# Performance work log

Hardware: AMD Instinct MI355X
Metric: run time of the kernel (lower is better)

The kernel has to match this reference:

```python
import jax, jax.numpy as jnp
import numpy as np

IM_SIZE = (32, 32)
SCALE = float(IM_SIZE[0] * IM_SIZE[1])  # sqrt((x*y)^2) = x*y


def setup_inputs() -> dict:
    key = jax.random.key(0)
    k1, k2, k3 = jax.random.split(key, 3)
    b, n, p, x, y, d = 8, 8, 64, IM_SIZE[0], IM_SIZE[1], 8
    shape = (b, n, p, x, y, d)
    return {
        "query": jax.random.normal(k1, shape, dtype=jnp.float32),
        "key": jax.random.normal(k2, shape, dtype=jnp.float32),
        "value": jax.random.normal(k3, shape, dtype=jnp.float32),
        "key_padding_mask": jnp.zeros((b, p), dtype=bool),
    }


def reference(query, key, value, key_padding_mask):
    # scores: contract over spatial (x,y) and channel (d) dims -> [b,n,p,q]
    scores = jnp.einsum('bnpxyd,bnqxyd->bnpq', query, key) / SCALE
    if key_padding_mask is not None:
        mask = key_padding_mask[:, None, None, :]  # [b,1,1,q]
        scores = jnp.where(mask, -jnp.inf, scores)
    attn = jax.nn.softmax(scores, axis=-1)  # [b,n,p,q]
    out = jnp.einsum('bnpq,bnqxyd->bnpxyd', attn, value)
    # permute(0,2,3,4,5,1) -> [b,p,x,y,d,n]
    return jnp.transpose(out, (0, 2, 3, 4, 5, 1))
```

## Files before the change

### kernel.cpp

```cpp
#include <hip/hip_runtime.h>
#include <hip/hip_bf16.h>
#include <cstdint>
#include <cstddef>


typedef __attribute__((ext_vector_type(4))) float f32x4;
typedef __attribute__((ext_vector_type(8))) short bf16x8;
typedef __attribute__((ext_vector_type(4))) short shortx4;

__device__ __forceinline__ unsigned short f2bf(float x) {
    unsigned int u = __builtin_bit_cast(unsigned int, x);
    u += 0x7FFFu + ((u >> 16) & 1u);
    return (unsigned short)(u >> 16);
}

#define BKK 32
#define LDS_STRIDE 68

__global__ __launch_bounds__(256) void qk_partial_kernel(
    const float* __restrict__ Q, const float* __restrict__ K,
    float* __restrict__ partial, int clen)
{
    __shared__ float As[BKK][LDS_STRIDE];
    __shared__ float Bs[BKK][LDS_STRIDE];
    const int bn  = blockIdx.x;
    const int ch  = blockIdx.y;
    const int tid = threadIdx.x;
    const float* Qb = Q + (size_t)bn * 64 * 8192;
    const float* Kb = K + (size_t)bn * 64 * 8192;
    const int k0 = ch * clen;

    const int lp  = tid >> 2;
    const int lk0 = (tid & 3) * 4;
    const int r0 = (tid >> 4) * 4;
    const int c0 = (tid & 15) * 4;

    float acc[4][4];
    #pragma unroll
    for (int i = 0; i < 4; ++i)
        #pragma unroll
        for (int j = 0; j < 4; ++j) acc[i][j] = 0.f;

    for (int kb = 0; kb < clen; kb += BKK) {
        const int kbase = k0 + kb;
        const float4 qa = *(const float4*)&Qb[(size_t)lp * 8192 + kbase + lk0];
        const float4 qc = *(const float4*)&Qb[(size_t)lp * 8192 + kbase + lk0 + 16];
        const float4 ka = *(const float4*)&Kb[(size_t)lp * 8192 + kbase + lk0];
        const float4 kc = *(const float4*)&Kb[(size_t)lp * 8192 + kbase + lk0 + 16];
        __syncthreads();
        As[lk0 + 0][lp] = qa.x;  As[lk0 + 1][lp] = qa.y;
        As[lk0 + 2][lp] = qa.z;  As[lk0 + 3][lp] = qa.w;
        As[lk0 + 16][lp] = qc.x; As[lk0 + 17][lp] = qc.y;
        As[lk0 + 18][lp] = qc.z; As[lk0 + 19][lp] = qc.w;
        Bs[lk0 + 0][lp] = ka.x;  Bs[lk0 + 1][lp] = ka.y;
        Bs[lk0 + 2][lp] = ka.z;  Bs[lk0 + 3][lp] = ka.w;
        Bs[lk0 + 16][lp] = kc.x; Bs[lk0 + 17][lp] = kc.y;
        Bs[lk0 + 18][lp] = kc.z; Bs[lk0 + 19][lp] = kc.w;
        __syncthreads();
        #pragma unroll
        for (int kk = 0; kk < BKK; ++kk) {
            const float4 av = *(const float4*)&As[kk][r0];
            const float4 bv = *(const float4*)&Bs[kk][c0];
            const float a4[4] = {av.x, av.y, av.z, av.w};
            const float b4[4] = {bv.x, bv.y, bv.z, bv.w};
            #pragma unroll
            for (int i = 0; i < 4; ++i)
                #pragma unroll
                for (int j = 0; j < 4; ++j)
                    acc[i][j] = fmaf(a4[i], b4[j], acc[i][j]);
        }
    }

    float* pb = partial + (((size_t)ch * 64 + bn) * 64) * 64;
    #pragma unroll
    for (int i = 0; i < 4; ++i) {
        float4 v;
        v.x = acc[i][0]; v.y = acc[i][1]; v.z = acc[i][2]; v.w = acc[i][3];
        *(float4*)&pb[(size_t)(r0 + i) * 64 + c0] = v;
    }
}

__global__ __launch_bounds__(256) void softmax_kernel(
    float* __restrict__ ws, const unsigned char* __restrict__ mask, int kchunks)
{
    const int row  = blockIdx.x * 4 + (threadIdx.x >> 6);
    const int q    = threadIdx.x & 63;
    float s = 0.f;
    for (int c = 0; c < kchunks; ++c)
        s += ws[((size_t)c * 4096 + row) * 64 + q];
    s *= (1.0f / 1024.0f);
    const int b = row >> 9;
    if (mask[b * 64 + q]) s = -__builtin_inff();
    float m = s;
    #pragma unroll
    for (int off = 32; off; off >>= 1) m = fmaxf(m, __shfl_xor(m, off));
    const float e = __expf(s - m);
    float sum = e;
    #pragma unroll
    for (int off = 32; off; off >>= 1) sum += __shfl_xor(sum, off);
    ws[(size_t)row * 64 + q] = e / sum;
}

__global__ __launch_bounds__(512, 2) void pv_mfma_kernel(
    const float* __restrict__ V, const float* __restrict__ attn,
    float* __restrict__ out)
{
    __shared__ unsigned char smem[65536];

    const int b     = blockIdx.y;
    const int chunk = blockIdx.x;
    const int tid   = threadIdx.x;
    const int w     = tid >> 6;
    const int lane  = tid & 63;

    const float* Vb = V    + (size_t)(b * 8 + w) * 64 * 8192 + (size_t)chunk * 64;
    const float* Ab = attn + (size_t)(b * 8 + w) * 4096;

    unsigned short* vtn = (unsigned short*)smem + w * 4096;

    const int c  = lane >> 2;
    const int qg = lane & 3;
    #pragma unroll
    for (int s = 0; s < 4; ++s) {
        const int q0 = s * 16 + qg * 4;
        const float4 r0 = *(const float4*)&Vb[(size_t)(q0 + 0) * 8192 + c * 4];
        const float4 r1 = *(const float4*)&Vb[(size_t)(q0 + 1) * 8192 + c * 4];
        const float4 r2 = *(const float4*)&Vb[(size_t)(q0 + 2) * 8192 + c * 4];
        const float4 r3 = *(const float4*)&Vb[(size_t)(q0 + 3) * 8192 + c * 4];
        const float v0[4] = {r0.x, r0.y, r0.z, r0.w};
        const float v1[4] = {r1.x, r1.y, r1.z, r1.w};
        const float v2[4] = {r2.x, r2.y, r2.z, r2.w};
        const float v3[4] = {r3.x, r3.y, r3.z, r3.w};
        #pragma unroll
        for (int cc = 0; cc < 4; ++cc) {
            const int row = c * 4 + cc;
            shortx4 pk;
            pk.x = (short)f2bf(v0[cc]);
            pk.y = (short)f2bf(v1[cc]);
            pk.z = (short)f2bf(v2[cc]);
            pk.w = (short)f2bf(v3[cc]);
            const int soff = row * 64 + (q0 ^ ((row & 7) << 3) ^ (((row >> 3) & 3) << 4));
            *(shortx4*)(vtn + soff) = pk;
        }
    }

    const int arow = lane & 15;
    const int q0a  = (lane >> 4) * 8;
    bf16x8 afrag[4][2];
    #pragma unroll
    for (int mt = 0; mt < 4; ++mt) {
        #pragma unroll
        for (int ks = 0; ks < 2; ++ks) {
            const float* ap = Ab + (mt * 16 + arow) * 64 + ks * 32 + q0a;
            const float4 lo = *(const float4*)ap;
            const float4 hi = *(const float4*)(ap + 4);
            bf16x8 f;
            f[0] = (short)f2bf(lo.x); f[1] = (short)f2bf(lo.y);
            f[2] = (short)f2bf(lo.z); f[3] = (short)f2bf(lo.w);
            f[4] = (short)f2bf(hi.x); f[5] = (short)f2bf(hi.y);
            f[6] = (short)f2bf(hi.z); f[7] = (short)f2bf(hi.w);
            afrag[mt][ks] = f;
        }
    }

    f32x4 acc[4][4];
    #pragma unroll
    for (int mt = 0; mt < 4; ++mt)
        #pragma unroll
        for (int nt = 0; nt < 4; ++nt)
            acc[mt][nt] = (f32x4)(0.f);

    const int bcol = lane & 15;
    const int q0b  = (lane >> 4) * 8;
    #pragma unroll
    for (int nt = 0; nt < 4; ++nt) {
        bf16x8 bfr[2];
        #pragma unroll
        for (int ks = 0; ks < 2; ++ks) {
            const int row  = nt * 16 + bcol;
            const int q0   = ks * 32 + q0b;
            const int soff = row * 64 + (q0 ^ ((row & 7) << 3) ^ (((row >> 3) & 3) << 4));
            bfr[ks] = *(const bf16x8*)(vtn + soff);
        }
        #pragma unroll
        for (int ks = 0; ks < 2; ++ks)
            #pragma unroll
            for (int mt = 0; mt < 4; ++mt)
                acc[mt][nt] = __builtin_amdgcn_mfma_f32_16x16x32_bf16(
                    afrag[mt][ks], bfr[ks], acc[mt][nt], 0, 0, 0);
    }

    float* ob = (float*)smem;
    const int pq = lane >> 4;
    const int pl = tid >> 5;
    const int g  = tid & 31;
    #pragma unroll
    for (int mt = 0; mt < 4; ++mt) {
        __syncthreads();
        #pragma unroll
        for (int nt = 0; nt < 4; ++nt)
            #pragma unroll
            for (int r = 0; r < 4; ++r) {
                const int prow = pq * 4 + r;
                const int xc   = nt * 16 + (lane & 15);
                ob[prow * 576 + xc * 9 + w] = acc[mt][nt][r];
            }
        __syncthreads();
        float* orow = out + (size_t)b * 4194304 + (size_t)(mt * 16 + pl) * 65536
                          + (size_t)chunk * 512;
        #pragma unroll
        for (int u = 0; u < 4; ++u) {
            const int f0 = g * 4 + u * 128;
            float4 vv;
            vv.x = ob[pl * 576 + ((f0 + 0) >> 3) * 9 + ((f0 + 0) & 7)];
            vv.y = ob[pl * 576 + ((f0 + 1) >> 3) * 9 + ((f0 + 1) & 7)];
            vv.z = ob[pl * 576 + ((f0 + 2) >> 3) * 9 + ((f0 + 2) & 7)];
            vv.w = ob[pl * 576 + ((f0 + 3) >> 3) * 9 + ((f0 + 3) & 7)];
            *(float4*)&orow[f0] = vv;
        }
    }
}

extern "C" void kernel_launch(void* const* d_in, const int* in_sizes, int n_in,
                              void* d_out, int out_size, void* d_ws, size_t ws_size,
                              hipStream_t stream)
{
    const float* Q = (const float*)d_in[0];
    const float* K = (const float*)d_in[1];
    const float* V = (const float*)d_in[2];
    const unsigned char* mask = (const unsigned char*)d_in[3];
    float* out = (float*)d_out;
    float* ws  = (float*)d_ws;

    int kchunks = 16;
    while (kchunks > 1 &&
           (size_t)kchunks * 4096 * 64 * sizeof(float) > ws_size)
        kchunks >>= 1;
    const int clen = 8192 / kchunks;

    qk_partial_kernel<<<dim3(64, kchunks), 256, 0, stream>>>(Q, K, ws, clen);
    softmax_kernel<<<1024, 256, 0, stream>>>(ws, mask, kchunks);
    pv_mfma_kernel<<<dim3(128, 8), 512, 0, stream>>>(V, ws, out);
}
```

Baseline: 150.0 us.

## Replace FP32 LDS-tiled QK GEMM with direct-load bf16 MFMA kernel

The QK score GEMM moves from scalar FP32 FMAs on LDS tiles to bf16 MFMA 16x16x32 instructions. Each wave loads its Q and K fragments straight from global memory, converting them to bf16 in registers, so there is no LDS staging and no barriers. This removes the scalar FMA compute bottleneck and the sync overhead. In exchange, scores are computed from bf16-rounded inputs (lower precision), and global reads are strided rows without LDS reuse, so Q and K fragments are loaded by two waves each.

```diff
diff --git a/kernel.cpp b/kernel.cpp
--- a/kernel.cpp
+++ b/kernel.cpp
@@ -14,70 +14,78 @@
     return (unsigned short)(u >> 16);
 }
 
-#define BKK 32
-#define LDS_STRIDE 68
-
-__global__ __launch_bounds__(256) void qk_partial_kernel(
+__global__ __launch_bounds__(256) void qk_mfma_kernel(
     const float* __restrict__ Q, const float* __restrict__ K,
     float* __restrict__ partial, int clen)
 {
-    __shared__ float As[BKK][LDS_STRIDE];
-    __shared__ float Bs[BKK][LDS_STRIDE];
-    const int bn  = blockIdx.x;
-    const int ch  = blockIdx.y;
-    const int tid = threadIdx.x;
-    const float* Qb = Q + (size_t)bn * 64 * 8192;
-    const float* Kb = K + (size_t)bn * 64 * 8192;
-    const int k0 = ch * clen;
-
-    const int lp  = tid >> 2;
-    const int lk0 = (tid & 3) * 4;
-    const int r0 = (tid >> 4) * 4;
-    const int c0 = (tid & 15) * 4;
-
-    float acc[4][4];
-    #pragma unroll
-    for (int i = 0; i < 4; ++i)
-        #pragma unroll
-        for (int j = 0; j < 4; ++j) acc[i][j] = 0.f;
-
-    for (int kb = 0; kb < clen; kb += BKK) {
-        const int kbase = k0 + kb;
-        const float4 qa = *(const float4*)&Qb[(size_t)lp * 8192 + kbase + lk0];
-        const float4 qc = *(const float4*)&Qb[(size_t)lp * 8192 + kbase + lk0 + 16];
-        const float4 ka = *(const float4*)&Kb[(size_t)lp * 8192 + kbase + lk0];
-        const float4 kc = *(const float4*)&Kb[(size_t)lp * 8192 + kbase + lk0 + 16];
-        __syncthreads();
-        As[lk0 + 0][lp] = qa.x;  As[lk0 + 1][lp] = qa.y;
-        As[lk0 + 2][lp] = qa.z;  As[lk0 + 3][lp] = qa.w;
-        As[lk0 + 16][lp] = qc.x; As[lk0 + 17][lp] = qc.y;
-        As[lk0 + 18][lp] = qc.z; As[lk0 + 19][lp] = qc.w;
-        Bs[lk0 + 0][lp] = ka.x;  Bs[lk0 + 1][lp] = ka.y;
-        Bs[lk0 + 2][lp] = ka.z;  Bs[lk0 + 3][lp] = ka.w;
-        Bs[lk0 + 16][lp] = kc.x; Bs[lk0 + 17][lp] = kc.y;
-        Bs[lk0 + 18][lp] = kc.z; Bs[lk0 + 19][lp] = kc.w;
-        __syncthreads();
-        #pragma unroll
-        for (int kk = 0; kk < BKK; ++kk) {
-            const float4 av = *(const float4*)&As[kk][r0];
-            const float4 bv = *(const float4*)&Bs[kk][c0];
-            const float a4[4] = {av.x, av.y, av.z, av.w};
-            const float b4[4] = {bv.x, bv.y, bv.z, bv.w};
-            #pragma unroll
-            for (int i = 0; i < 4; ++i)
-                #pragma unroll
-                for (int j = 0; j < 4; ++j)
-                    acc[i][j] = fmaf(a4[i], b4[j], acc[i][j]);
-        }
-    }
-
-    float* pb = partial + (((size_t)ch * 64 + bn) * 64) * 64;
-    #pragma unroll
-    for (int i = 0; i < 4; ++i) {
-        float4 v;
-        v.x = acc[i][0]; v.y = acc[i][1]; v.z = acc[i][2]; v.w = acc[i][3];
-        *(float4*)&pb[(size_t)(r0 + i) * 64 + c0] = v;
-    }
+    const int bn   = blockIdx.x;
+    const int ch   = blockIdx.y;
+    const int tid  = threadIdx.x;
+    const int w    = tid >> 6;
+    const int lane = tid & 63;
+    const int wr   = w >> 1;
+    const int wc   = w & 1;
+    const int frow = lane & 15;
+    const int kg   = lane >> 4;
+
+    const float* Qb = Q + (size_t)bn * 64 * 8192 + (size_t)ch * clen;
+    const float* Kb = K + (size_t)bn * 64 * 8192 + (size_t)ch * clen;
+    const float* Aq = Qb + (size_t)(wr * 32 + frow) * 8192 + kg * 8;
+    const float* Bk = Kb + (size_t)(wc * 32 + frow) * 8192 + kg * 8;
+
+    f32x4 acc[2][2];
+    #pragma unroll
+    for (int mt = 0; mt < 2; ++mt)
+        #pragma unroll
+        for (int nt = 0; nt < 2; ++nt)
+            acc[mt][nt] = (f32x4)(0.f);
+
+    #pragma unroll 2
+    for (int ks = 0; ks < clen; ks += 32) {
+        bf16x8 afr[2], bfr[2];
+        #pragma unroll
+        for (int mt = 0; mt < 2; ++mt) {
+            const float* p = Aq + (size_t)mt * 16 * 8192 + ks;
+            const float4 lo = *(const float4*)p;
+            const float4 hi = *(const float4*)(p + 4);
+            bf16x8 f;
+            f[0] = (short)f2bf(lo.x); f[1] = (short)f2bf(lo.y);
+            f[2] = (short)f2bf(lo.z); f[3] = (short)f2bf(lo.w);
+            f[4] = (short)f2bf(hi.x); f[5] = (short)f2bf(hi.y);
+            f[6] = (short)f2bf(hi.z); f[7] = (short)f2bf(hi.w);
+            afr[mt] = f;
+        }
+        #pragma unroll
+        for (int nt = 0; nt < 2; ++nt) {
+            const float* p = Bk + (size_t)nt * 16 * 8192 + ks;
+            const float4 lo = *(const float4*)p;
+            const float4 hi = *(const float4*)(p + 4);
+            bf16x8 f;
+            f[0] = (short)f2bf(lo.x); f[1] = (short)f2bf(lo.y);
+            f[2] = (short)f2bf(lo.z); f[3] = (short)f2bf(lo.w);
+            f[4] = (short)f2bf(hi.x); f[5] = (short)f2bf(hi.y);
+            f[6] = (short)f2bf(hi.z); f[7] = (short)f2bf(hi.w);
+            bfr[nt] = f;
+        }
+        #pragma unroll
+        for (int mt = 0; mt < 2; ++mt)
+            #pragma unroll
+            for (int nt = 0; nt < 2; ++nt)
+                acc[mt][nt] = __builtin_amdgcn_mfma_f32_16x16x32_bf16(
+                    afr[mt], bfr[nt], acc[mt][nt], 0, 0, 0);
+    }
+
+    float* pb = partial + ((size_t)ch * 64 + bn) * 4096;
+    #pragma unroll
+    for (int mt = 0; mt < 2; ++mt)
+        #pragma unroll
+        for (int nt = 0; nt < 2; ++nt) {
+            const int p0 = wr * 32 + mt * 16 + kg * 4;
+            const int q0 = wc * 32 + nt * 16 + frow;
+            #pragma unroll
+            for (int r = 0; r < 4; ++r)
+                pb[(size_t)(p0 + r) * 64 + q0] = acc[mt][nt][r];
+        }
 }
 
 __global__ __launch_bounds__(256) void softmax_kernel(
@@ -238,7 +246,7 @@
         kchunks >>= 1;
     const int clen = 8192 / kchunks;
 
-    qk_partial_kernel<<<dim3(64, kchunks), 256, 0, stream>>>(Q, K, ws, clen);
+    qk_mfma_kernel<<<dim3(64, kchunks), 256, 0, stream>>>(Q, K, ws, clen);
     softmax_kernel<<<1024, 256, 0, stream>>>(ws, mask, kchunks);
     pv_mfma_kernel<<<dim3(128, 8), 512, 0, stream>>>(V, ws, out);
 }
```

New measurement: 152.5 us. About the same (+1.7%).
